# Optimization experiments

Measured on AMD Instinct MI355X. Metric: run time of the kernel, lower is better.

Reference implementation:

```python
import jax, jax.numpy as jnp
import numpy as np

N_NODES = 100000


def _lightgcn_layer(x, src, dst, norm):
    # message: norm * x[src]; aggregate: mean over incoming edges at dst
    msg = norm[:, None] * x[src]                                   # [E+N, D]
    s = jax.ops.segment_sum(msg, dst, num_segments=N_NODES)        # [N, D]
    cnt = jax.ops.segment_sum(jnp.ones_like(norm), dst, num_segments=N_NODES)
    return s / cnt[:, None]                                        # deg>=1 due to self-loops


def _graph_embeddings(emb, edge_index):
    n = emb.shape[0]
    loop = jnp.arange(n, dtype=edge_index.dtype)
    src = jnp.concatenate([edge_index[0], loop])                   # self-loops appended
    dst = jnp.concatenate([edge_index[1], loop])
    deg = jax.ops.segment_sum(jnp.ones(src.shape[0], emb.dtype), src, num_segments=N_NODES)
    dis = deg ** -0.5
    norm = dis[src] * dis[dst]
    x = emb
    acc = emb
    for _ in range(2):  # num_layers
        x = _lightgcn_layer(x, src, dst, norm)
        acc = acc + x
    return acc / 3.0  # mean over (num_layers + 1) embeddings


def setup_inputs() -> dict:
    key = jax.random.key(0)
    k1, k2, k3, k4 = jax.random.split(key, 4)
    emb = jax.random.normal(k1, (N_NODES, 128), dtype=jnp.float32) * 0.02
    edge_index = jax.random.randint(k2, (2, 600000), 0, N_NODES, dtype=jnp.int64)
    items = jax.random.randint(k3, (4096, 1), 0, N_NODES, dtype=jnp.int64)
    samples = jax.random.randint(k4, (4096, 100), 0, N_NODES, dtype=jnp.int64)
    return {"emb": emb, "edge_index": edge_index, "items": items, "samples": samples}


def reference(emb, edge_index, items, samples):
    embeddings = _graph_embeddings(emb, edge_index)                # [N, D]
    item_emb = embeddings[items]                                   # [B, 1, D]
    sample_emb = embeddings[samples]                               # [B, S, D]
    scores = jnp.einsum('bod,bsd->bos', item_emb, sample_emb)      # [B, 1, S]
    return scores.squeeze(1)                                       # [B, S]
```

## Files before the change

kernel.cpp:

```cpp
#include <hip/hip_runtime.h>

#define NN 100000
#define D 128
#define W 32
#define EPT 2

__device__ __forceinline__ unsigned short f2bf(float f) {
    unsigned u = __float_as_uint(f);
    u += 0x7FFF + ((u >> 16) & 1);
    return (unsigned short)(u >> 16);
}
__device__ __forceinline__ float bflo(unsigned u) { return __uint_as_float(u << 16); }
__device__ __forceinline__ float bfhi(unsigned u) { return __uint_as_float(u & 0xFFFF0000u); }
__device__ __forceinline__ unsigned pack2(float a, float b) {
    return (unsigned)f2bf(a) | ((unsigned)f2bf(b) << 16);
}
__device__ __forceinline__ void addrow(float* acc, const uint4 v, float w) {
    acc[0] += w * bflo(v.x); acc[1] += w * bfhi(v.x);
    acc[2] += w * bflo(v.y); acc[3] += w * bfhi(v.y);
    acc[4] += w * bflo(v.z); acc[5] += w * bfhi(v.z);
    acc[6] += w * bflo(v.w); acc[7] += w * bfhi(v.w);
}

__global__ __launch_bounds__(256) void hetero_kernel(const int* __restrict__ src,
                                                     const int* __restrict__ dst,
                                                     const float* __restrict__ emb,
                                                     int* __restrict__ deg,
                                                     int* __restrict__ fillc,
                                                     int* __restrict__ ell,
                                                     unsigned short* __restrict__ y0h,
                                                     int E, int EB, int total, int total8) {
    int b = blockIdx.x;
    int lo = (int)(((long long)b * EB) / total);
    int hi = (int)(((long long)(b + 1) * EB) / total);
    if (hi > lo) {
        int e0 = lo * (256 * EPT) + threadIdx.x;
        int e1 = e0 + 256;
        int sa = -1, sb = -1, da = 0, db = 0;
        if (e0 < E) { sa = src[e0]; da = dst[e0]; }
        if (e1 < E) { sb = src[e1]; db = dst[e1]; }
        if (sa >= 0) atomicAdd(&deg[sa], 1);
        if (sb >= 0) atomicAdd(&deg[sb], 1);
        int pa = -1, pb = -1;
        if (sa >= 0) pa = atomicAdd(&fillc[da], 1);
        if (sb >= 0) pb = atomicAdd(&fillc[db], 1);
        if (sa >= 0 && pa < W) ell[(size_t)da * W + pa] = sa;
        if (sb >= 0 && pb < W) ell[(size_t)db * W + pb] = sb;
    } else {
        int t = (b - hi) * 256 + threadIdx.x;
        if (t < total8) {
            const float4 a = ((const float4*)emb)[t * 2];
            const float4 c = ((const float4*)emb)[t * 2 + 1];
            uint4 o;
            o.x = pack2(a.x, a.y);
            o.y = pack2(a.z, a.w);
            o.z = pack2(c.x, c.y);
            o.w = pack2(c.z, c.w);
            ((uint4*)y0h)[t] = o;
        }
    }
}

__global__ __launch_bounds__(256) void gather1_kernel(const int* __restrict__ ell,
                                                      const int* __restrict__ fillc,
                                                      const int* __restrict__ deg,
                                                      const unsigned short* __restrict__ y0h,
                                                      unsigned short* __restrict__ y1h, int n) {
    unsigned t = blockIdx.x * 256u + threadIdx.x;
    unsigned i = t >> 4, q = t & 15u;
    if (i >= (unsigned)n) return;
    int len = fillc[i];
    int lenc = len > W ? W : len;
    const int* base = ell + (size_t)i * W;
    float wd = rsqrtf((float)deg[i] + 1.0f);
    const uint4 ph = *(const uint4*)(y0h + (size_t)i * D + q * 8);
    float acc[8] = {0.f, 0.f, 0.f, 0.f, 0.f, 0.f, 0.f, 0.f};
    addrow(acc, ph, wd);
    int j = 0;
    for (; j + 4 <= lenc; j += 4) {
        const int4 ss = *(const int4*)(base + j);
        float w0 = rsqrtf((float)deg[ss.x] + 1.0f);
        float w1 = rsqrtf((float)deg[ss.y] + 1.0f);
        float w2 = rsqrtf((float)deg[ss.z] + 1.0f);
        float w3 = rsqrtf((float)deg[ss.w] + 1.0f);
        const uint4 v0 = *(const uint4*)(y0h + (size_t)ss.x * D + q * 8);
        const uint4 v1 = *(const uint4*)(y0h + (size_t)ss.y * D + q * 8);
        const uint4 v2 = *(const uint4*)(y0h + (size_t)ss.z * D + q * 8);
        const uint4 v3 = *(const uint4*)(y0h + (size_t)ss.w * D + q * 8);
        addrow(acc, v0, w0);
        addrow(acc, v1, w1);
        addrow(acc, v2, w2);
        addrow(acc, v3, w3);
    }
    for (; j < lenc; ++j) {
        int s0 = base[j];
        float w0 = rsqrtf((float)deg[s0] + 1.0f);
        const uint4 v0 = *(const uint4*)(y0h + (size_t)s0 * D + q * 8);
        addrow(acc, v0, w0);
    }
    float ci = 1.0f / (float)(len + 1);
    float f1 = ci * wd * wd;
    uint4 o;
    o.x = pack2(f1 * acc[0], f1 * acc[1]);
    o.y = pack2(f1 * acc[2], f1 * acc[3]);
    o.z = pack2(f1 * acc[4], f1 * acc[5]);
    o.w = pack2(f1 * acc[6], f1 * acc[7]);
    *(uint4*)(y1h + (size_t)i * D + q * 8) = o;
}

__global__ __launch_bounds__(256) void gather2_kernel(const int* __restrict__ ell,
                                                      const int* __restrict__ fillc,
                                                      const int* __restrict__ deg,
                                                      const unsigned short* __restrict__ y1h,
                                                      const unsigned short* __restrict__ y0h,
                                                      unsigned short* __restrict__ finh, int n) {
    unsigned t = blockIdx.x * 256u + threadIdx.x;
    unsigned i = t >> 4, q = t & 15u;
    if (i >= (unsigned)n) return;
    int len = fillc[i];
    int lenc = len > W ? W : len;
    const int* base = ell + (size_t)i * W;
    const uint4 ph = *(const uint4*)(y1h + (size_t)i * D + q * 8);
    const uint4 pe = *(const uint4*)(y0h + (size_t)i * D + q * 8);
    float self[8];
    self[0] = bflo(ph.x); self[1] = bfhi(ph.x);
    self[2] = bflo(ph.y); self[3] = bfhi(ph.y);
    self[4] = bflo(ph.z); self[5] = bfhi(ph.z);
    self[6] = bflo(ph.w); self[7] = bfhi(ph.w);
    float acc[8];
    #pragma unroll
    for (int k = 0; k < 8; ++k) acc[k] = self[k];
    int j = 0;
    for (; j + 4 <= lenc; j += 4) {
        const int4 ss = *(const int4*)(base + j);
        const uint4 v0 = *(const uint4*)(y1h + (size_t)ss.x * D + q * 8);
        const uint4 v1 = *(const uint4*)(y1h + (size_t)ss.y * D + q * 8);
        const uint4 v2 = *(const uint4*)(y1h + (size_t)ss.z * D + q * 8);
        const uint4 v3 = *(const uint4*)(y1h + (size_t)ss.w * D + q * 8);
        addrow(acc, v0, 1.0f);
        addrow(acc, v1, 1.0f);
        addrow(acc, v2, 1.0f);
        addrow(acc, v3, 1.0f);
    }
    for (; j < lenc; ++j) {
        int s0 = base[j];
        const uint4 v0 = *(const uint4*)(y1h + (size_t)s0 * D + q * 8);
        addrow(acc, v0, 1.0f);
    }
    float dp1 = (float)deg[i] + 1.0f;
    float wd = rsqrtf(dp1);
    float wdi = sqrtf(dp1);
    float ci = 1.0f / (float)(len + 1);
    float g = ci * wd;
    const float k3 = 1.0f / 3.0f;
    float e[8];
    e[0] = bflo(pe.x); e[1] = bfhi(pe.x);
    e[2] = bflo(pe.y); e[3] = bfhi(pe.y);
    e[4] = bflo(pe.z); e[5] = bfhi(pe.z);
    e[6] = bflo(pe.w); e[7] = bfhi(pe.w);
    float r[8];
    #pragma unroll
    for (int k = 0; k < 8; ++k) r[k] = (e[k] + self[k] * wdi + g * acc[k]) * k3;
    uint4 o;
    o.x = pack2(r[0], r[1]);
    o.y = pack2(r[2], r[3]);
    o.z = pack2(r[4], r[5]);
    o.w = pack2(r[6], r[7]);
    *(uint4*)(finh + (size_t)i * D + q * 8) = o;
}

__global__ __launch_bounds__(256) void scores_kernel(const unsigned short* __restrict__ finh,
                                                     const int* __restrict__ items,
                                                     const int* __restrict__ samples,
                                                     float* __restrict__ out, int S) {
    __shared__ float it[D];
    int b = blockIdx.x;
    if (threadIdx.x < 64) {
        unsigned u = ((const unsigned*)(finh + (size_t)items[b] * D))[threadIdx.x];
        it[threadIdx.x * 2] = bflo(u);
        it[threadIdx.x * 2 + 1] = bfhi(u);
    }
    __syncthreads();
    int g = threadIdx.x >> 4, lane = threadIdx.x & 15;
    float w[8];
    #pragma unroll
    for (int k = 0; k < 8; ++k) w[k] = it[lane * 8 + k];
    int s = g;
    for (; s + 16 < S; s += 32) {
        int node0 = samples[b * S + s];
        int node1 = samples[b * S + s + 16];
        const uint4 v0 = *(const uint4*)(finh + (size_t)node0 * D + lane * 8);
        const uint4 v1 = *(const uint4*)(finh + (size_t)node1 * D + lane * 8);
        float a0 = w[0] * bflo(v0.x) + w[1] * bfhi(v0.x) + w[2] * bflo(v0.y) + w[3] * bfhi(v0.y)
                 + w[4] * bflo(v0.z) + w[5] * bfhi(v0.z) + w[6] * bflo(v0.w) + w[7] * bfhi(v0.w);
        float a1 = w[0] * bflo(v1.x) + w[1] * bfhi(v1.x) + w[2] * bflo(v1.y) + w[3] * bfhi(v1.y)
                 + w[4] * bflo(v1.z) + w[5] * bfhi(v1.z) + w[6] * bflo(v1.w) + w[7] * bfhi(v1.w);
        #pragma unroll
        for (int o = 8; o; o >>= 1) {
            a0 += __shfl_xor(a0, o);
            a1 += __shfl_xor(a1, o);
        }
        if (lane == 0) {
            out[b * S + s] = a0;
            out[b * S + s + 16] = a1;
        }
    }
    if (s < S) {
        int node = samples[b * S + s];
        const uint4 v = *(const uint4*)(finh + (size_t)node * D + lane * 8);
        float a = w[0] * bflo(v.x) + w[1] * bfhi(v.x) + w[2] * bflo(v.y) + w[3] * bfhi(v.y)
                + w[4] * bflo(v.z) + w[5] * bfhi(v.z) + w[6] * bflo(v.w) + w[7] * bfhi(v.w);
        #pragma unroll
        for (int o = 8; o; o >>= 1) a += __shfl_xor(a, o);
        if (lane == 0) out[b * S + s] = a;
    }
}

extern "C" void kernel_launch(void* const* d_in, const int* in_sizes, int n_in,
                              void* d_out, int out_size, void* d_ws, size_t ws_size,
                              hipStream_t stream) {
    const float* emb = (const float*)d_in[0];
    const int* ei = (const int*)d_in[1];
    const int* items = (const int*)d_in[2];
    const int* samples = (const int*)d_in[3];
    float* out = (float*)d_out;

    const int E = in_sizes[1] / 2;
    const int B = in_sizes[2];
    const int S = in_sizes[3] / B;
    const int* src = ei;
    const int* dst = ei + E;

    int* deg = (int*)d_ws;
    int* fillc = deg + NN;
    int* ell = fillc + NN;
    unsigned short* y0h = (unsigned short*)(ell + (size_t)NN * W);
    unsigned short* y1h = y0h + (size_t)NN * D;
    unsigned short* finh = y1h + (size_t)NN * D;

    hipMemsetAsync(deg, 0, 2 * NN * sizeof(int), stream);

    const int EB = (E + 256 * EPT - 1) / (256 * EPT);
    const int total8 = NN * D / 8;
    const int CB = (total8 + 255) / 256;
    const int total = EB + CB;
    hetero_kernel<<<total, 256, 0, stream>>>(src, dst, emb, deg, fillc, ell, y0h,
                                             E, EB, total, total8);

    const int gblocks = (NN * 16 + 255) / 256;
    gather1_kernel<<<gblocks, 256, 0, stream>>>(ell, fillc, deg, y0h, y1h, NN);
    gather2_kernel<<<gblocks, 256, 0, stream>>>(ell, fillc, deg, y1h, y0h, finh, NN);

    scores_kernel<<<B, 256, 0, stream>>>(finh, items, samples, out, S);
}
```

Baseline: 150.3 us.

## Compute source degrees with LDS-privatized packed histograms instead of global atomics

Out-degree counting moves out of the edge-scatter kernel into a separate LDS histogram kernel. It uses 128 blocks, each covering half the node range and a 1/64 slice of the edges, with two 16-bit counters packed per word. A reduction kernel then sums the 64 partial histograms into deg. This removes 600k global atomics from the hetero kernel. In exchange it adds two launches, an extra pass over src, and about 12.8MB of partial-histogram traffic. The 16-bit counters could overflow on heavily skewed graphs, though not on these random inputs.

```diff
diff --git a/kernel.cpp b/kernel.cpp
--- a/kernel.cpp
+++ b/kernel.cpp
@@ -4,6 +4,9 @@
 #define D 128
 #define W 32
 #define EPT 2
+#define HRS 50000
+#define HWORDS 25000
+#define HSPLIT 64
 
 __device__ __forceinline__ unsigned short f2bf(float f) {
     unsigned u = __float_as_uint(f);
@@ -22,10 +25,38 @@
     acc[6] += w * bflo(v.w); acc[7] += w * bfhi(v.w);
 }
 
+__global__ __launch_bounds__(256) void hist1_kernel(const int* __restrict__ src,
+                                                    unsigned* __restrict__ part, int E) {
+    __shared__ unsigned h[HWORDS];
+    int r = blockIdx.x >> 6, c = blockIdx.x & (HSPLIT - 1);
+    for (int t = threadIdx.x; t < HWORDS; t += 256) h[t] = 0;
+    __syncthreads();
+    int chunk = (E + HSPLIT - 1) / HSPLIT;
+    int e0 = c * chunk, e1 = min(e0 + chunk, E);
+    int lo = r * HRS;
+    for (int e = e0 + (int)threadIdx.x; e < e1; e += 256) {
+        unsigned s = (unsigned)(src[e] - lo);
+        if (s < (unsigned)HRS) atomicAdd(&h[s >> 1], 1u << ((s & 1u) << 4));
+    }
+    __syncthreads();
+    unsigned* dstp = part + (size_t)c * (2 * HWORDS) + (size_t)r * HWORDS;
+    for (int t = threadIdx.x; t < HWORDS; t += 256) dstp[t] = h[t];
+}
+
+__global__ __launch_bounds__(256) void histB_kernel(const unsigned* __restrict__ part,
+                                                    int* __restrict__ deg, int nw) {
+    int w = blockIdx.x * 256 + threadIdx.x;
+    if (w >= nw) return;
+    unsigned s = 0;
+    #pragma unroll
+    for (int c = 0; c < HSPLIT; ++c) s += part[(size_t)c * (2 * HWORDS) + w];
+    deg[2 * w] = (int)(s & 0xFFFFu);
+    deg[2 * w + 1] = (int)(s >> 16);
+}
+
 __global__ __launch_bounds__(256) void hetero_kernel(const int* __restrict__ src,
                                                      const int* __restrict__ dst,
                                                      const float* __restrict__ emb,
-                                                     int* __restrict__ deg,
                                                      int* __restrict__ fillc,
                                                      int* __restrict__ ell,
                                                      unsigned short* __restrict__ y0h,
@@ -39,8 +70,6 @@
         int sa = -1, sb = -1, da = 0, db = 0;
         if (e0 < E) { sa = src[e0]; da = dst[e0]; }
         if (e1 < E) { sb = src[e1]; db = dst[e1]; }
-        if (sa >= 0) atomicAdd(&deg[sa], 1);
-        if (sb >= 0) atomicAdd(&deg[sb], 1);
         int pa = -1, pb = -1;
         if (sa >= 0) pa = atomicAdd(&fillc[da], 1);
         if (sb >= 0) pb = atomicAdd(&fillc[db], 1);
@@ -234,18 +263,23 @@
     int* deg = (int*)d_ws;
     int* fillc = deg + NN;
     int* ell = fillc + NN;
-    unsigned short* y0h = (unsigned short*)(ell + (size_t)NN * W);
+    unsigned* part = (unsigned*)(ell + (size_t)NN * W);
+    unsigned short* y0h = (unsigned short*)(part + (size_t)HSPLIT * 2 * HWORDS);
     unsigned short* y1h = y0h + (size_t)NN * D;
     unsigned short* finh = y1h + (size_t)NN * D;
 
-    hipMemsetAsync(deg, 0, 2 * NN * sizeof(int), stream);
+    hipMemsetAsync(fillc, 0, NN * sizeof(int), stream);
+
+    hist1_kernel<<<2 * HSPLIT, 256, 0, stream>>>(src, part, E);
 
     const int EB = (E + 256 * EPT - 1) / (256 * EPT);
     const int total8 = NN * D / 8;
     const int CB = (total8 + 255) / 256;
     const int total = EB + CB;
-    hetero_kernel<<<total, 256, 0, stream>>>(src, dst, emb, deg, fillc, ell, y0h,
+    hetero_kernel<<<total, 256, 0, stream>>>(src, dst, emb, fillc, ell, y0h,
                                              E, EB, total, total8);
+
+    histB_kernel<<<(2 * HWORDS + 255) / 256, 256, 0, stream>>>(part, deg, 2 * HWORDS);
 
     const int gblocks = (NN * 16 + 255) / 256;
     gather1_kernel<<<gblocks, 256, 0, stream>>>(ell, fillc, deg, y0h, y1h, NN);
```

Result: no change. 151.5 us (+0.8%).
